# Performance work log

Hardware: AMD Instinct MI355X
Metric: run time of the kernel (lower is better)

## Reference

```python
import jax, jax.numpy as jnp
import numpy as np

B, T, W, H, F = 256, 128, 32, 512, 1024


def setup_inputs() -> dict:
    key = jax.random.key(0)
    ks = jax.random.split(key, 8)
    s = 0.05
    return {
        "inputs": jax.random.normal(ks[0], (B, T, 2), jnp.float32),
        "Wk": jax.random.normal(ks[1], (2, 4 * H), jnp.float32) * s,
        "Wr": jax.random.normal(ks[2], (H, 4 * H), jnp.float32) * s,
        "b": jnp.zeros((4 * H,), jnp.float32),
        "Ww": jax.random.normal(ks[3], (H, 2), jnp.float32) * s,
        "bw": jnp.zeros((2,), jnp.float32),
        "Wc": jax.random.normal(ks[4], (2, H), jnp.float32) * s,
        "bc": jnp.zeros((H,), jnp.float32),
        "Wcc": jax.random.normal(ks[5], (W * H, F), jnp.float32) * s,
        "bcc": jnp.zeros((F,), jnp.float32),
        "Wp": jax.random.normal(ks[6], (F, 2), jnp.float32) * s,
        "bp": jnp.zeros((2,), jnp.float32),
        "Wco": jax.random.normal(ks[7], (F, 1), jnp.float32) * s,
        "bco": jnp.zeros((1,), jnp.float32),
    }


def _cell(x, h, c, Wk, Wr, b):
    # Keras LSTMCell: gate order i, f, g(candidate), o; sigmoid recurrent act, tanh act.
    z = x @ Wk + h @ Wr + b
    i, f, g, o = jnp.split(z, 4, axis=-1)
    c = jax.nn.sigmoid(f) * c + jax.nn.sigmoid(i) * jnp.tanh(g)
    h = jax.nn.sigmoid(o) * jnp.tanh(c)
    return h, c


def reference(inputs, Wk, Wr, b, Ww, bw, Wc, bc, Wcc, bcc, Wp, bp, Wco, bco):
    # Masking(-1.0) is a no-op for Gaussian inputs; dropout is identity at inference.
    warm_seq = jnp.swapaxes(inputs[:, W:], 0, 1)  # [T-W, B, 2]
    h0 = jnp.zeros((inputs.shape[0], H), inputs.dtype)
    c0 = jnp.zeros_like(h0)

    def warm_step(carry, x):
        h, c = carry
        h, c = _cell(x, h, c, Wk, Wr, b)
        return (h, c), None

    (h, c), _ = jax.lax.scan(warm_step, (h0, c0), warm_seq)
    warm_out = h  # warm_up_lstm_output, [B, H]
    pred0 = h @ Ww + bw  # dense_warm (linear activation), [B, 2]

    def dec_step(carry, _):
        h, c, pred = carry
        h, c = _cell(pred, h, c, Wk, Wr, b)
        pred = h @ Ww + bw
        return (h, c, pred), pred

    n_dec = T - W - 1  # range(1, time - warm_up_length)
    _, preds_rest = jax.lax.scan(dec_step, (h, c, pred0), None, length=n_dec)
    predictions = jnp.concatenate([pred0[None], preds_rest], axis=0)  # [T-W, B, 2]
    predictions = jnp.swapaxes(predictions, 0, 1)  # [B, T-W, 2]

    cand = jax.nn.relu(inputs[:, : W - 1] @ Wc + bc)  # [B, W-1, H]
    cand = cand.reshape(cand.shape[0], -1)  # flatten -> [B, (W-1)*H]
    cat = jnp.concatenate([warm_out, cand], axis=1)  # [B, W*H]
    ct = jax.nn.relu(cat @ Wcc + bcc)  # dense_concat, [B, F]
    candidate_prob = jax.nn.sigmoid(ct @ Wp + bp)  # [B, 2]
    candidate_cost = ct @ Wco + bco  # [B, 1]
    return predictions, candidate_cost, candidate_prob, inputs
```

## Files before the change

kernel.cpp:

```cpp
#include <hip/hip_runtime.h>
#include <hip/hip_bf16.h>
#include <stdint.h>

#define B_    256
#define T_    128
#define W_    32
#define H_    512
#define G4_   2048
#define TW_   96
#define STEPS_ 191
#define TEAMS 16
#define MEMBERS 16
#define ROWS  16
#define HC    32

typedef __attribute__((ext_vector_type(8))) short short8;
typedef __attribute__((ext_vector_type(4))) float f32x4;
typedef __attribute__((ext_vector_type(4))) uint32_t u32x4;

__device__ __forceinline__ unsigned short f2bf(float f) {
  uint32_t u = __float_as_uint(f);
  u += 0x7fffu + ((u >> 16) & 1u);
  return (unsigned short)(u >> 16);
}
__device__ __forceinline__ float sigm(float x) { return 1.f / (1.f + __expf(-x)); }
__device__ __forceinline__ float tanh_(float x) { return 1.f - 2.f / (1.f + __expf(2.f * x)); }

#define LOAD_CF(p)      __hip_atomic_load((p), __ATOMIC_RELAXED, __HIP_MEMORY_SCOPE_AGENT)
#define LOAD_CI(p)      __hip_atomic_load((p), __ATOMIC_RELAXED, __HIP_MEMORY_SCOPE_AGENT)
#define ARRIVE(p)       __hip_atomic_fetch_add((p), 1, __ATOMIC_RELAXED, __HIP_MEMORY_SCOPE_AGENT)

__device__ __forceinline__ u32x4 ld16c(const void* p) {
  u32x4 v;
  asm volatile("global_load_dwordx4 %0, %1, off sc0 sc1"
               : "=&v"(v) : "v"(p) : "memory");
  return v;
}
__device__ __forceinline__ void st16c(void* p, u32x4 v) {
  asm volatile("global_store_dwordx4 %0, %1, off sc0 sc1" :: "v"(p), "v"(v) : "memory");
}
__device__ __forceinline__ void stf16c(void* p, f32x4 v) {
  asm volatile("global_store_dwordx4 %0, %1, off sc0 sc1" :: "v"(p), "v"(v) : "memory");
}

__global__ __launch_bounds__(256, 1) void lstm_kernel(
    const float* __restrict__ inputs, const float* __restrict__ Wk,
    const float* __restrict__ Wr, const float* __restrict__ bias,
    const float* __restrict__ Ww, const float* __restrict__ bw,
    const float* __restrict__ Wc, const float* __restrict__ bc,
    const float* __restrict__ Wcc,
    unsigned short* __restrict__ h0buf, unsigned short* __restrict__ h1buf,
    float* __restrict__ pp0, float* __restrict__ pp1,
    unsigned short* __restrict__ warm, int* __restrict__ flags,
    float* __restrict__ partialT, float* __restrict__ out_pred)
{
  const int team = blockIdx.x & 15;
  const int member = blockIdx.x >> 4;
  const int rbase = team * ROWS;
  const int hbase = member * HC;
  const int tid = threadIdx.x;
  const int wave = tid >> 6;
  const int lane = tid & 63;
  const int l4 = lane >> 4, l16 = lane & 15;

  __shared__ unsigned short h_lds[ROWS][H_];
  __shared__ float x_all[TW_][ROWS][2];
  __shared__ float x_lds[ROWS][2];
  __shared__ float pp_lds[4][ROWS][2];
  __shared__ alignas(16) unsigned short h_out[ROWS][HC];
  __shared__ float wc0[512], wc1[512], bcl[512];
  __shared__ float xin[256][10];

  const int kc = blockIdx.x >> 5, gnc = blockIdx.x & 31;
  const int koff = (kc == 0) ? 0 : kc*2048 - 512;
  const int nks  = (kc == 0) ? 48 : 64;
  const int gw0 = koff >> 9;

  for (int i = tid; i < TW_*ROWS*2; i += 256) {
    int tt = i >> 5, row = (i >> 1) & 15, c = i & 1;
    x_all[tt][row][c] = inputs[(size_t)(rbase+row)*(T_*2) + (W_+tt)*2 + c];
  }
  for (int i = tid; i < 512; i += 256) {
    wc0[i] = Wc[i]; wc1[i] = Wc[512 + i]; bcl[i] = bc[i];
  }
  for (int i = tid; i < 2560; i += 256) {
    int row = i / 10, r = i - row*10;
    xin[row][r] = inputs[(size_t)row*(T_*2) + gw0*2 + r];
  }

  const int gateL = l16 & 3, hclL = l16 >> 2;
  short8 afrag[2][16];
  float bbv[2][4], wk0v[2][4], wk1v[2][4], wwv[2][2];
#pragma unroll
  for (int a = 0; a < 2; a++) {
    const int gcA = gateL*H_ + hbase + wave*8 + a*4 + hclL;
#pragma unroll
    for (int ks = 0; ks < 16; ks++) {
      const float* wp = Wr + (size_t)(ks*32 + l4*8) * G4_ + gcA;
#pragma unroll
      for (int j = 0; j < 8; j++) afrag[a][ks][j] = (short)f2bf(wp[(size_t)j * G4_]);
    }
    const int colA = hbase + wave*8 + a*4 + l4;
#pragma unroll
    for (int j = 0; j < 4; j++) {
      int gcj = j*H_ + colA;
      bbv[a][j] = bias[gcj]; wk0v[a][j] = Wk[gcj]; wk1v[a][j] = Wk[G4_ + gcj];
    }
    wwv[a][0] = Ww[2*colA]; wwv[a][1] = Ww[2*colA + 1];
  }
  const float bwc0 = bw[0], bwc1 = bw[1];
  float creg[2] = {0.f, 0.f};

  const int nhalf = wave & 1, bhalf = wave >> 1;
  const int gnrow = gnc*32 + nhalf*16 + l16;
  f32x4 gacc[8];
#pragma unroll
  for (int i = 0; i < 8; i++) gacc[i] = (f32x4){0.f,0.f,0.f,0.f};
  float fn[8];
  {
    const float* wp = Wcc + (size_t)(512 + koff + l4*8) * 1024 + gnrow;
#pragma unroll
    for (int j = 0; j < 8; j++) fn[j] = wp[(size_t)j * 1024];
  }
  int gq = 0, gphase = 0;
  __syncthreads();

  int* ctr = flags + team * 16;
  const int srow = tid >> 4, sg = tid & 15;

  for (int t = 0; t < STEPS_; t++) {
    const unsigned short* hprev = (t & 1) ? h1buf : h0buf;
    unsigned short* hnext = (t & 1) ? h0buf : h1buf;
    const float* ppprev = (t & 1) ? pp1 : pp0;
    float* ppnext = (t & 1) ? pp0 : pp1;

    const bool dox = (t >= TW_) && (tid < 32);
    float vals[MEMBERS];
    if (dox) {
      int row = tid >> 1, c = tid & 1;
      const float* pps = ppprev + (size_t)team*MEMBERS*32 + row*2 + c;
#pragma unroll
      for (int m = 0; m < MEMBERS; m++) vals[m] = LOAD_CF(pps + m*32);
    }
    u32x4 q[4];
    {
      const unsigned short* srcb = hprev + (size_t)(rbase+srow)*H_ + sg*8;
#pragma unroll
      for (int i = 0; i < 4; i++) q[i] = ld16c(srcb + i*128);
    }
    asm volatile("s_waitcnt vmcnt(0)" ::: "memory");
    __builtin_amdgcn_sched_barrier(0);
#pragma unroll
    for (int i = 0; i < 4; i++)
      *(u32x4*)&h_lds[srow][((sg + 16*i) ^ (srow & 7)) * 8] = q[i];
    if (dox) {
      int row = tid >> 1, c = tid & 1;
      float s = c ? bwc1 : bwc0;
#pragma unroll
      for (int m = 0; m < MEMBERS; m++) s += vals[m];
      x_lds[row][c] = s;
      if (member == 0)
        out_pred[((size_t)(rbase+row)*96 + (t - TW_))*2 + c] = s;
    }
    __syncthreads();

    f32x4 acc[2];
    const float* xsrc = (t < TW_) ? &x_all[t][0][0] : &x_lds[0][0];
    {
      float x0 = xsrc[2*l16], x1 = xsrc[2*l16 + 1];
#pragma unroll
      for (int a = 0; a < 2; a++)
#pragma unroll
        for (int j = 0; j < 4; j++)
          acc[a][j] = bbv[a][j] + wk0v[a][j]*x0 + wk1v[a][j]*x1;
    }
#pragma unroll
    for (int ks = 0; ks < 16; ks++) {
      int pg = ((ks*4 + l4) ^ (l16 & 7)) * 8;
      short8 b0 = *(const short8*)&h_lds[l16][pg];
      acc[0] = __builtin_amdgcn_mfma_f32_16x16x32_bf16(afrag[0][ks], b0, acc[0], 0,0,0);
      acc[1] = __builtin_amdgcn_mfma_f32_16x16x32_bf16(afrag[1][ks], b0, acc[1], 0,0,0);
    }

    float pp0v = 0.f, pp1v = 0.f;
#pragma unroll
    for (int a = 0; a < 2; a++) {
      float zi = acc[a][0], zf = acc[a][1], zg = acc[a][2], zo = acc[a][3];
      float cn = sigm(zf)*creg[a] + sigm(zi)*tanh_(zg);
      float hn = sigm(zo)*tanh_(cn);
      creg[a] = cn;
      pp0v += hn * wwv[a][0];
      pp1v += hn * wwv[a][1];
      h_out[l16][wave*8 + a*4 + l4] = f2bf(hn);
    }
    if (t >= TW_ - 1) {
      pp0v += __shfl_xor(pp0v, 16); pp0v += __shfl_xor(pp0v, 32);
      pp1v += __shfl_xor(pp1v, 16); pp1v += __shfl_xor(pp1v, 32);
      if (l4 == 0) {
        pp_lds[wave][l16][0] = pp0v;
        pp_lds[wave][l16][1] = pp1v;
      }
    }
    __syncthreads();

    if (tid < 64) {
      int row = tid >> 2, qd = tid & 3;
      u32x4 v = *(const u32x4*)&h_out[row][qd*8];
      st16c(hnext + (size_t)(rbase+row)*H_ + hbase + qd*8, v);
      if (t == TW_ - 1)
        *(u32x4*)(warm + (size_t)(rbase+row)*H_ + hbase + qd*8) = v;
    }
    if (t >= TW_ - 1 && tid < 8) {
      f32x4 pv;
#pragma unroll
      for (int j = 0; j < 4; j++) {
        int idx = tid*4 + j, row = idx >> 1, c = idx & 1;
        pv[j] = pp_lds[0][row][c] + pp_lds[1][row][c]
              + pp_lds[2][row][c] + pp_lds[3][row][c];
      }
      stf16c(ppnext + (size_t)(team*MEMBERS + member)*32 + tid*4, pv);
    }

    asm volatile("s_waitcnt vmcnt(0)" ::: "memory");
    __syncthreads();
    if (tid == 0) ARRIVE(ctr);

    if (gphase == 0 && gq < nks) {
      const int kkl = koff + gq*32 + l4*8;
      short8 af;
#pragma unroll
      for (int j = 0; j < 8; j++) af[j] = (short)f2bf(fn[j]);
      if (gq + 1 < nks) {
        const float* wp = Wcc + (size_t)(512 + kkl + 32) * 1024 + gnrow;
#pragma unroll
        for (int j = 0; j < 8; j++) fn[j] = wp[(size_t)j * 1024];
      }
      const int w = kkl >> 9, hc = kkl & 511;
      const int wi = (w - gw0)*2;
      float c0[8], c1[8], cb[8];
#pragma unroll
      for (int j = 0; j < 8; j++) {
        c0[j] = wc0[hc+j]; c1[j] = wc1[hc+j]; cb[j] = bcl[hc+j];
      }
#pragma unroll
      for (int bt = 0; bt < 8; bt++) {
        int row = bhalf*128 + bt*16 + l16;
        float x0 = xin[row][wi], x1 = xin[row][wi+1];
        short8 bf;
#pragma unroll
        for (int j = 0; j < 8; j++) {
          float v = fmaf(x0, c0[j], fmaf(x1, c1[j], cb[j]));
          bf[j] = (short)f2bf(fmaxf(v, 0.f));
        }
        gacc[bt] = __builtin_amdgcn_mfma_f32_16x16x32_bf16(af, bf, gacc[bt], 0,0,0);
      }
      gq++;
    }
    gphase = (gphase == 2) ? 0 : gphase + 1;

    if (tid == 0) {
      int need = MEMBERS * (t + 1);
      while (LOAD_CI(ctr) < need) {}
    }
    __syncthreads();
  }

  if (member == 0 && tid < 32) {
    int row = tid >> 1, c = tid & 1;
    const float* pps = pp1 + (size_t)team*MEMBERS*32 + row*2 + c;
    float s = c ? bwc1 : bwc0;
#pragma unroll
    for (int m = 0; m < MEMBERS; m++) s += LOAD_CF(pps + m*32);
    out_pred[((size_t)(rbase+row)*96 + 95)*2 + c] = s;
  }

  {
    float* pp = partialT + (size_t)kc*262144
              + (size_t)(gnc*32 + nhalf*16 + l4*4)*256 + bhalf*128 + l16;
#pragma unroll
    for (int bt = 0; bt < 8; bt++)
#pragma unroll
      for (int r = 0; r < 4; r++)
        pp[(size_t)r*256 + bt*16] = gacc[bt][r];
  }
}

__global__ __launch_bounds__(256, 1) void gemm0_kernel(
    const unsigned short* __restrict__ warm, const float* __restrict__ Wcc,
    float* __restrict__ partial8)
{
  const int nc = blockIdx.x;
  const int tid = threadIdx.x;
  const int w = tid >> 6, lane = tid & 63;
  const int l4 = lane >> 4, l16 = lane & 15;

  f32x4 zero = {0.f,0.f,0.f,0.f};
  f32x4 acc[16];
#pragma unroll
  for (int i = 0; i < 16; i++) acc[i] = zero;

  const int nrow = nc*64 + w*16 + l16;
  for (int ks = 0; ks < 16; ks++) {
    const float* wp = Wcc + (size_t)(ks*32 + l4*8) * 1024 + nrow;
    short8 af;
#pragma unroll
    for (int j = 0; j < 8; j++) af[j] = (short)f2bf(wp[(size_t)j * 1024]);
    const unsigned short* cp = warm + ks*32 + l4*8;
#pragma unroll
    for (int bt = 0; bt < 16; bt++) {
      short8 bf = *(const short8*)(cp + (size_t)(bt*16 + l16) * 512);
      acc[bt] = __builtin_amdgcn_mfma_f32_16x16x32_bf16(af, bf, acc[bt], 0,0,0);
    }
  }
  float* pp = partial8 + (size_t)(nc*64 + w*16 + l4*4)*256 + l16;
#pragma unroll
  for (int bt = 0; bt < 16; bt++)
#pragma unroll
    for (int r = 0; r < 4; r++)
      pp[(size_t)r*256 + bt*16] = acc[bt][r];
}

__global__ void reduce_kernel(const float* __restrict__ partialT,
                              const float* __restrict__ partial8,
                              const float* __restrict__ bcc, float* __restrict__ ctT,
                              const float* __restrict__ inputs, float* __restrict__ out)
{
  int e = blockIdx.x * 256 + threadIdx.x;
  int n = e >> 8;
  float s = bcc[n] + partial8[e];
#pragma unroll
  for (int p = 0; p < 8; p++) s += partialT[(size_t)p*262144 + e];
  ctT[e] = fmaxf(s, 0.f);
  if (e < 65536) out[49920 + e] = inputs[e];
}

__global__ void head_kernel(const float* __restrict__ ctT, const float* __restrict__ Wp,
                            const float* __restrict__ bp, const float* __restrict__ Wco,
                            const float* __restrict__ bco, float* __restrict__ out)
{
  int b = blockIdx.x;
  int lane = threadIdx.x;
  float p0 = 0.f, p1 = 0.f, pc = 0.f;
#pragma unroll
  for (int i = 0; i < 16; i++) {
    int n = i*64 + lane;
    float c = ctT[(size_t)n*256 + b];
    p0 += c * Wp[2*n]; p1 += c * Wp[2*n+1]; pc += c * Wco[n];
  }
  for (int m = 1; m < 64; m <<= 1) {
    p0 += __shfl_xor(p0, m); p1 += __shfl_xor(p1, m); pc += __shfl_xor(pc, m);
  }
  if (lane == 0) {
    out[49152 + b]       = pc + bco[0];
    out[49408 + 2*b]     = 1.f / (1.f + __expf(-(p0 + bp[0])));
    out[49408 + 2*b + 1] = 1.f / (1.f + __expf(-(p1 + bp[1])));
  }
}

extern "C" void kernel_launch(void* const* d_in, const int* in_sizes, int n_in,
                              void* d_out, int out_size, void* d_ws, size_t ws_size,
                              hipStream_t stream) {
  const float* inputs = (const float*)d_in[0];
  const float* Wk   = (const float*)d_in[1];
  const float* Wr   = (const float*)d_in[2];
  const float* bias = (const float*)d_in[3];
  const float* Ww   = (const float*)d_in[4];
  const float* bw   = (const float*)d_in[5];
  const float* Wc   = (const float*)d_in[6];
  const float* bc   = (const float*)d_in[7];
  const float* Wcc  = (const float*)d_in[8];
  const float* bcc  = (const float*)d_in[9];
  const float* Wp   = (const float*)d_in[10];
  const float* bp   = (const float*)d_in[11];
  const float* Wco  = (const float*)d_in[12];
  const float* bco  = (const float*)d_in[13];
  float* out = (float*)d_out;
  char* ws = (char*)d_ws;

  unsigned short* h0   = (unsigned short*)(ws);
  int*            flags= (int*)(ws + 0x40000);
  unsigned short* h1   = (unsigned short*)(ws + 0x42000);
  unsigned short* warm = (unsigned short*)(ws + 0x82000);
  float*          pp0  = (float*)(ws + 0xC2000);
  float*          pp1  = (float*)(ws + 0xCA000);
  float*          partial8 = (float*)(ws + 0xD2000);
  float*          partialT = (float*)(ws + 0x8C2000);
  float*          ctT  = (float*)(ws + 0x10C2000);

  hipMemsetAsync(d_ws, 0, 0x42000, stream);

  lstm_kernel<<<TEAMS*MEMBERS, 256, 0, stream>>>(inputs, Wk, Wr, bias, Ww, bw,
                                                 Wc, bc, Wcc,
                                                 h0, h1, pp0, pp1, warm, flags,
                                                 partialT, out);
  gemm0_kernel<<<16, 256, 0, stream>>>(warm, Wcc, partial8);
  reduce_kernel<<<1024, 256, 0, stream>>>(partialT, partial8, bcc, ctT, inputs, out);
  head_kernel<<<256, 64, 0, stream>>>(ctT, Wp, bp, Wco, bco, out);
}
```

Before: 652.9 us.

## Fold warm-state GEMM into LSTM kernel and spread concat GEMM across steps

Removes the separate gemm0 kernel by having the kc==0 blocks consume the warm hidden state inside the persistent LSTM kernel, gated by a global counter that all blocks bump after the warm-up step. The dense_concat GEMM work is now split into half-chunks placed in the latency gaps around the h-load and the inter-block barrier, on alternating steps, instead of one full chunk every third step. This is meant to hide the GEMM under the recurrent loop's synchronisation stalls and drop one kernel launch plus the partial8 round trip. The cost is a spin-wait on all 256 blocks for the kc==0 group and extra instructions in the latency-critical recurrent step.

New measurement: 634.2 us, median of 2. 1.03x faster.

```diff
diff --git a/kernel.cpp b/kernel.cpp
--- a/kernel.cpp
+++ b/kernel.cpp
@@ -42,6 +42,48 @@
 __device__ __forceinline__ void stf16c(void* p, f32x4 v) {
   asm volatile("global_store_dwordx4 %0, %1, off sc0 sc1" :: "v"(p), "v"(v) : "memory");
 }
+
+#define GBT_RELU(C0, C1)                                                      \
+  {                                                                           \
+    const int kkl_ = gK - 512 + l4*8;                                         \
+    const int hc_ = kkl_ & 511;                                               \
+    const int wi_ = ((kkl_ >> 9) - gw0) * 2;                                  \
+    {                                                                         \
+      int row_ = bhalf*128 + (C0)*16 + l16;                                   \
+      float x0_ = xin[row_][wi_], x1_ = xin[row_][wi_+1];                     \
+      short8 bf_;                                                             \
+      _Pragma("unroll")                                                       \
+      for (int j = 0; j < 8; j++) {                                           \
+        float v_ = fmaf(x0_, wc0[hc_+j], fmaf(x1_, wc1[hc_+j], bcl[hc_+j]));  \
+        bf_[j] = (short)f2bf(fmaxf(v_, 0.f));                                 \
+      }                                                                       \
+      gacc[C0] = __builtin_amdgcn_mfma_f32_16x16x32_bf16(af, bf_, gacc[C0], 0,0,0); \
+    }                                                                         \
+    {                                                                         \
+      int row_ = bhalf*128 + (C1)*16 + l16;                                   \
+      float x0_ = xin[row_][wi_], x1_ = xin[row_][wi_+1];                     \
+      short8 bf_;                                                             \
+      _Pragma("unroll")                                                       \
+      for (int j = 0; j < 8; j++) {                                           \
+        float v_ = fmaf(x0_, wc0[hc_+j], fmaf(x1_, wc1[hc_+j], bcl[hc_+j]));  \
+        bf_[j] = (short)f2bf(fmaxf(v_, 0.f));                                 \
+      }                                                                       \
+      gacc[C1] = __builtin_amdgcn_mfma_f32_16x16x32_bf16(af, bf_, gacc[C1], 0,0,0); \
+    }                                                                         \
+  }
+
+#define GBT_WARM(C0, C1)                                                      \
+  {                                                                           \
+    const unsigned short* wb_ = warm + gK + l4*8;                             \
+    u32x4 wv0_ = ld16c(wb_ + (size_t)(bhalf*128 + (C0)*16 + l16) * 512);      \
+    u32x4 wv1_ = ld16c(wb_ + (size_t)(bhalf*128 + (C1)*16 + l16) * 512);      \
+    asm volatile("s_waitcnt vmcnt(0)" ::: "memory");                          \
+    __builtin_amdgcn_sched_barrier(0);                                        \
+    short8 b0_ = *(const short8*)&wv0_;                                       \
+    short8 b1_ = *(const short8*)&wv1_;                                       \
+    gacc[C0] = __builtin_amdgcn_mfma_f32_16x16x32_bf16(af, b0_, gacc[C0], 0,0,0); \
+    gacc[C1] = __builtin_amdgcn_mfma_f32_16x16x32_bf16(af, b1_, gacc[C1], 0,0,0); \
+  }
 
 __global__ __launch_bounds__(256, 1) void lstm_kernel(
     const float* __restrict__ inputs, const float* __restrict__ Wk,
@@ -72,9 +114,8 @@
   __shared__ float xin[256][10];
 
   const int kc = blockIdx.x >> 5, gnc = blockIdx.x & 31;
-  const int koff = (kc == 0) ? 0 : kc*2048 - 512;
-  const int nks  = (kc == 0) ? 48 : 64;
-  const int gw0 = koff >> 9;
+  const bool iskc0 = (kc == 0);
+  const int gw0 = iskc0 ? 0 : kc*4 - 1;
 
   for (int i = tid; i < TW_*ROWS*2; i += 256) {
     int tt = i >> 5, row = (i >> 1) & 15, c = i & 1;
@@ -111,21 +152,26 @@
   const float bwc0 = bw[0], bwc1 = bw[1];
   float creg[2] = {0.f, 0.f};
 
+  auto KIDX = [&](int g) -> int {
+    return iskc0 ? (g < 48 ? 512 + g*32 : (g - 48)*32) : kc*2048 + g*32;
+  };
   const int nhalf = wave & 1, bhalf = wave >> 1;
   const int gnrow = gnc*32 + nhalf*16 + l16;
   f32x4 gacc[8];
 #pragma unroll
   for (int i = 0; i < 8; i++) gacc[i] = (f32x4){0.f,0.f,0.f,0.f};
+  short8 af;
   float fn[8];
   {
-    const float* wp = Wcc + (size_t)(512 + koff + l4*8) * 1024 + gnrow;
+    const float* wp = Wcc + (size_t)(KIDX(0) + l4*8) * 1024 + gnrow;
 #pragma unroll
     for (int j = 0; j < 8; j++) fn[j] = wp[(size_t)j * 1024];
   }
-  int gq = 0, gphase = 0;
+  int gq = -1, gK = 0, phase = 1;
   __syncthreads();
 
   int* ctr = flags + team * 16;
+  int* gctr2 = flags + 256;
   const int srow = tid >> 4, sg = tid & 15;
 
   for (int t = 0; t < STEPS_; t++) {
@@ -147,6 +193,10 @@
       const unsigned short* srcb = hprev + (size_t)(rbase+srow)*H_ + sg*8;
 #pragma unroll
       for (int i = 0; i < 4; i++) q[i] = ld16c(srcb + i*128);
+    }
+    if (gq >= 0 && gq < 64) {
+      if (gK < 512) { if (!phase) GBT_WARM(0,1) else GBT_WARM(4,5) }
+      else          { if (!phase) GBT_RELU(0,1) else GBT_RELU(4,5) }
     }
     asm volatile("s_waitcnt vmcnt(0)" ::: "memory");
     __builtin_amdgcn_sched_barrier(0);
@@ -208,7 +258,7 @@
       u32x4 v = *(const u32x4*)&h_out[row][qd*8];
       st16c(hnext + (size_t)(rbase+row)*H_ + hbase + qd*8, v);
       if (t == TW_ - 1)
-        *(u32x4*)(warm + (size_t)(rbase+row)*H_ + hbase + qd*8) = v;
+        st16c(warm + (size_t)(rbase+row)*H_ + hbase + qd*8, v);
     }
     if (t >= TW_ - 1 && tid < 8) {
       f32x4 pv;
@@ -223,41 +273,34 @@
 
     asm volatile("s_waitcnt vmcnt(0)" ::: "memory");
     __syncthreads();
-    if (tid == 0) ARRIVE(ctr);
-
-    if (gphase == 0 && gq < nks) {
-      const int kkl = koff + gq*32 + l4*8;
-      short8 af;
-#pragma unroll
-      for (int j = 0; j < 8; j++) af[j] = (short)f2bf(fn[j]);
-      if (gq + 1 < nks) {
-        const float* wp = Wcc + (size_t)(512 + kkl + 32) * 1024 + gnrow;
-#pragma unroll
-        for (int j = 0; j < 8; j++) fn[j] = wp[(size_t)j * 1024];
+    if (tid == 0) {
+      ARRIVE(ctr);
+      if (t == TW_ - 1) ARRIVE(gctr2);
+    }
+    if (gq >= 0 && gq < 64) {
+      if (gK < 512) { if (!phase) GBT_WARM(2,3) else GBT_WARM(6,7) }
+      else          { if (!phase) GBT_RELU(2,3) else GBT_RELU(6,7) }
+    }
+    if (phase) {
+      if (gq + 1 < 64) {
+        gq++;
+        gK = KIDX(gq);
+#pragma unroll
+        for (int j = 0; j < 8; j++) af[j] = (short)f2bf(fn[j]);
+        if (iskc0 && gq == 48) {
+          if (tid == 0) { while (LOAD_CI(gctr2) < 256) {} }
+          __syncthreads();
+        }
+        if (gq + 1 < 64) {
+          const float* wp = Wcc + (size_t)(KIDX(gq + 1) + l4*8) * 1024 + gnrow;
+#pragma unroll
+          for (int j = 0; j < 8; j++) fn[j] = wp[(size_t)j * 1024];
+        }
+      } else {
+        gq = 64;
       }
-      const int w = kkl >> 9, hc = kkl & 511;
-      const int wi = (w - gw0)*2;
-      float c0[8], c1[8], cb[8];
-#pragma unroll
-      for (int j = 0; j < 8; j++) {
-        c0[j] = wc0[hc+j]; c1[j] = wc1[hc+j]; cb[j] = bcl[hc+j];
-      }
-#pragma unroll
-      for (int bt = 0; bt < 8; bt++) {
-        int row = bhalf*128 + bt*16 + l16;
-        float x0 = xin[row][wi], x1 = xin[row][wi+1];
-        short8 bf;
-#pragma unroll
-        for (int j = 0; j < 8; j++) {
-          float v = fmaf(x0, c0[j], fmaf(x1, c1[j], cb[j]));
-          bf[j] = (short)f2bf(fmaxf(v, 0.f));
-        }
-        gacc[bt] = __builtin_amdgcn_mfma_f32_16x16x32_bf16(af, bf, gacc[bt], 0,0,0);
-      }
-      gq++;
-    }
-    gphase = (gphase == 2) ? 0 : gphase + 1;
-
+    }
+    phase ^= 1;
     if (tid == 0) {
       int need = MEMBERS * (t + 1);
       while (LOAD_CI(ctr) < need) {}
@@ -285,49 +328,13 @@
   }
 }
 
-__global__ __launch_bounds__(256, 1) void gemm0_kernel(
-    const unsigned short* __restrict__ warm, const float* __restrict__ Wcc,
-    float* __restrict__ partial8)
-{
-  const int nc = blockIdx.x;
-  const int tid = threadIdx.x;
-  const int w = tid >> 6, lane = tid & 63;
-  const int l4 = lane >> 4, l16 = lane & 15;
-
-  f32x4 zero = {0.f,0.f,0.f,0.f};
-  f32x4 acc[16];
-#pragma unroll
-  for (int i = 0; i < 16; i++) acc[i] = zero;
-
-  const int nrow = nc*64 + w*16 + l16;
-  for (int ks = 0; ks < 16; ks++) {
-    const float* wp = Wcc + (size_t)(ks*32 + l4*8) * 1024 + nrow;
-    short8 af;
-#pragma unroll
-    for (int j = 0; j < 8; j++) af[j] = (short)f2bf(wp[(size_t)j * 1024]);
-    const unsigned short* cp = warm + ks*32 + l4*8;
-#pragma unroll
-    for (int bt = 0; bt < 16; bt++) {
-      short8 bf = *(const short8*)(cp + (size_t)(bt*16 + l16) * 512);
-      acc[bt] = __builtin_amdgcn_mfma_f32_16x16x32_bf16(af, bf, acc[bt], 0,0,0);
-    }
-  }
-  float* pp = partial8 + (size_t)(nc*64 + w*16 + l4*4)*256 + l16;
-#pragma unroll
-  for (int bt = 0; bt < 16; bt++)
-#pragma unroll
-    for (int r = 0; r < 4; r++)
-      pp[(size_t)r*256 + bt*16] = acc[bt][r];
-}
-
 __global__ void reduce_kernel(const float* __restrict__ partialT,
-                              const float* __restrict__ partial8,
                               const float* __restrict__ bcc, float* __restrict__ ctT,
                               const float* __restrict__ inputs, float* __restrict__ out)
 {
   int e = blockIdx.x * 256 + threadIdx.x;
   int n = e >> 8;
-  float s = bcc[n] + partial8[e];
+  float s = bcc[n];
 #pragma unroll
   for (int p = 0; p < 8; p++) s += partialT[(size_t)p*262144 + e];
   ctT[e] = fmaxf(s, 0.f);
@@ -383,7 +390,6 @@
   unsigned short* warm = (unsigned short*)(ws + 0x82000);
   float*          pp0  = (float*)(ws + 0xC2000);
   float*          pp1  = (float*)(ws + 0xCA000);
-  float*          partial8 = (float*)(ws + 0xD2000);
   float*          partialT = (float*)(ws + 0x8C2000);
   float*          ctT  = (float*)(ws + 0x10C2000);
 
@@ -393,7 +399,6 @@
                                                  Wc, bc, Wcc,
                                                  h0, h1, pp0, pp1, warm, flags,
                                                  partialT, out);
-  gemm0_kernel<<<16, 256, 0, stream>>>(warm, Wcc, partial8);
-  reduce_kernel<<<1024, 256, 0, stream>>>(partialT, partial8, bcc, ctT, inputs, out);
+  reduce_kernel<<<1024, 256, 0, stream>>>(partialT, bcc, ctT, inputs, out);
   head_kernel<<<256, 64, 0, stream>>>(ctT, Wp, bp, Wco, bco, out);
 }
```
